# Kernel tuning notes

Hardware: AMD Instinct MI355X
Metric: run time of the kernel (lower is better)

Reference implementation:

```python
import jax, jax.numpy as jnp
import numpy as np

N = 100000
E = 3200000
IN_C, HID_C, OUT_C = 602, 256, 41
K = 10
ALPHA = 0.1
CLIP = 1000000.0


def _ntn(x):
    return jnp.nan_to_num(x, nan=0.0, posinf=CLIP, neginf=-CLIP)


def setup_inputs() -> dict:
    key = jax.random.key(0)
    k1, k2, k3, k4, k5 = jax.random.split(key, 5)
    x = jax.random.normal(k1, (N, IN_C), dtype=jnp.float32)
    edge_index = jax.random.randint(k2, (2, E), 0, N, dtype=jnp.int32)
    # Xavier-uniform linear weights (torch Linear: y = x @ W.T + b)
    lim1 = float(np.sqrt(6.0 / (IN_C + HID_C)))
    lim2 = float(np.sqrt(6.0 / (HID_C + OUT_C)))
    W1 = jax.random.uniform(k3, (HID_C, IN_C), jnp.float32, -lim1, lim1)
    W2 = jax.random.uniform(k4, (OUT_C, HID_C), jnp.float32, -lim2, lim2)
    b1 = jnp.zeros((HID_C,), jnp.float32)
    b2 = jnp.zeros((OUT_C,), jnp.float32)
    return {"x": x, "edge_index": edge_index, "W1": W1, "b1": b1, "W2": W2, "b2": b2}


def reference(x, edge_index, W1, b1, W2, b2):
    # MLP encoder (eval mode: dropout is identity)
    h = _ntn(x)
    h = jax.nn.relu(h @ W1.T + b1)
    h = _ntn(h)
    h = h @ W2.T + b2
    h = _ntn(h)

    # is_reddit path: L2-normalize rows before propagation
    h = h / jnp.maximum(jnp.linalg.norm(h, axis=1, keepdims=True), 1e-12)

    # APPNP with GCN normalization and added self-loops
    self_loop = jnp.arange(N, dtype=edge_index.dtype)
    row = jnp.concatenate([edge_index[0], self_loop])  # sources
    col = jnp.concatenate([edge_index[1], self_loop])  # targets
    deg = jax.ops.segment_sum(jnp.ones_like(col, dtype=h.dtype), col, num_segments=N)
    dinv = jax.lax.rsqrt(deg)  # deg >= 1 with self-loops
    norm = dinv[row] * dinv[col]  # [E+N]

    h0 = h

    def step(h_k, _):
        msg = h_k[row] * norm[:, None]  # gather + scale
        agg = jax.ops.segment_sum(msg, col, num_segments=N)  # scatter-add
        return (1.0 - ALPHA) * agg + ALPHA * h0, None

    out, _ = jax.lax.scan(step, h, None, length=K)
    out = _ntn(out)  # nan_to_num after prop (reddit path) and final nan_to_num
    return out
```

## Files before the change

kernel.cpp:

```cpp
#include <hip/hip_runtime.h>

#define N_NODES 100000
#define N_EDGES 3200000
#define IN_C 602
#define KPAD 608
#define NT 19
#define HID_C 256
#define OUTC 41
#define HSTR 64
#define K_ITERS 10
#define NBUK 391
#define NBLK_BIN 256
#define CHUNK 12500

typedef __attribute__((ext_vector_type(8))) short bf16x8;
typedef __attribute__((ext_vector_type(4))) float f32x4;

static __device__ __forceinline__ unsigned short f2bf(float f) {
  unsigned u = __float_as_uint(f);
  u += 0x7fffu + ((u >> 16) & 1u);
  return (unsigned short)(u >> 16);
}
static __device__ __forceinline__ float bf2f(unsigned short h) {
  return __uint_as_float(((unsigned)h) << 16);
}
static __device__ __forceinline__ float bflo(unsigned u) {
  return __uint_as_float(u << 16);
}
static __device__ __forceinline__ float bfhi(unsigned u) {
  return __uint_as_float(u & 0xffff0000u);
}
static __device__ __forceinline__ unsigned enc8(float v) {
  return (unsigned)(int)rintf(fminf(fmaxf(v * 127.f + 128.f, 0.f), 255.f));
}
static __device__ __forceinline__ unsigned pk4(float a, float b, float c, float d) {
  return enc8(a) | (enc8(b) << 8) | (enc8(c) << 16) | (enc8(d) << 24);
}

__global__ __launch_bounds__(256) void dinv_kernel(const unsigned* __restrict__ offs,
                                                   float* __restrict__ dinv) {
  int i = blockIdx.x * 256 + threadIdx.x;
  if (i < N_NODES) dinv[i] = rsqrtf((float)(offs[i + 1] - offs[i] + 1u));
}

__global__ __launch_bounds__(256) void binA_kernel(const int* __restrict__ col,
                                                   unsigned* __restrict__ gh) {
  __shared__ unsigned lh[NBUK];
  const int tid = threadIdx.x, blk = blockIdx.x;
  for (int i = tid; i < NBUK; i += 256) lh[i] = 0;
  __syncthreads();
  const int start = blk * CHUNK;
  const int end = (start + CHUNK < N_EDGES) ? start + CHUNK : N_EDGES;
  for (int e = start + tid; e < end; e += 256)
    atomicAdd(&lh[col[e] >> 8], 1u);
  __syncthreads();
  for (int i = tid; i < NBUK; i += 256)
    gh[(size_t)i * NBLK_BIN + blk] = lh[i];
}

__global__ __launch_bounds__(512) void binScan_kernel(unsigned* __restrict__ gh,
                                                      unsigned* __restrict__ bbase2,
                                                      unsigned* __restrict__ bhist) {
  __shared__ unsigned wsum[8];
  __shared__ unsigned wbase[8];
  const int t = threadIdx.x, lane = t & 63, w = t >> 6;
  unsigned tot = 0;
  if (t < NBUK) {
    unsigned* gp = gh + (size_t)t * NBLK_BIN;
#pragma unroll 8
    for (int j = 0; j < NBLK_BIN; ++j) tot += gp[j];
  }
  unsigned inc = tot;
  for (int d = 1; d < 64; d <<= 1) {
    unsigned x = (unsigned)__shfl_up((int)inc, d);
    if (lane >= d) inc += x;
  }
  if (lane == 63) wsum[w] = inc;
  __syncthreads();
  if (t == 0) {
    unsigned run = 0;
    for (int i = 0; i < 8; ++i) { unsigned s = wsum[i]; wbase[i] = run; run += s; }
  }
  __syncthreads();
  if (t < NBUK) {
    unsigned base = wbase[w] + inc - tot;
    bbase2[t] = base;
    bhist[t] = tot;
    unsigned* gp = gh + (size_t)t * NBLK_BIN;
    unsigned run = base;
#pragma unroll 8
    for (int j = 0; j < NBLK_BIN; ++j) {
      unsigned v = gp[j];
      gp[j] = run;
      run += v;
    }
  }
}

__global__ __launch_bounds__(256) void binB_kernel(const int* __restrict__ row,
                                                   const int* __restrict__ col,
                                                   const unsigned* __restrict__ gh,
                                                   unsigned* __restrict__ binned) {
  __shared__ unsigned lbase[NBUK];
  __shared__ unsigned lcur[NBUK];
  const int tid = threadIdx.x, blk = blockIdx.x;
  for (int i = tid; i < NBUK; i += 256) {
    lbase[i] = gh[(size_t)i * NBLK_BIN + blk];
    lcur[i] = 0;
  }
  __syncthreads();
  const int start = blk * CHUNK;
  const int end = (start + CHUNK < N_EDGES) ? start + CHUNK : N_EDGES;
  for (int e = start + tid; e < end; e += 256) {
    int r = row[e], c = col[e];
    int b = c >> 8;
    unsigned idx = atomicAdd(&lcur[b], 1u);
    binned[lbase[b] + idx] = (((unsigned)(c & 255)) << 17) | (unsigned)r;
  }
}

__global__ __launch_bounds__(256) void place_kernel(const unsigned* __restrict__ binned,
                                                    const unsigned* __restrict__ bbase2,
                                                    const unsigned* __restrict__ bhist,
                                                    unsigned* __restrict__ offs,
                                                    unsigned* __restrict__ rec4) {
  __shared__ unsigned lcnt[256];
  __shared__ unsigned lbase[256];
  __shared__ unsigned lcur[256];
  __shared__ unsigned wsum[4];
  __shared__ unsigned wbase[4];
  const int tid = threadIdx.x, lane = tid & 63, w = tid >> 6;
  const int b = blockIdx.x;
  const unsigned s = bbase2[b];
  const unsigned cnt = bhist[b];
  lcnt[tid] = 0;
  __syncthreads();
  for (unsigned i = tid; i < cnt; i += 256)
    atomicAdd(&lcnt[binned[s + i] >> 17], 1u);
  __syncthreads();
  unsigned v = lcnt[tid];
  unsigned inc = v;
  for (int d = 1; d < 64; d <<= 1) {
    unsigned x = (unsigned)__shfl_up((int)inc, d);
    if (lane >= d) inc += x;
  }
  if (lane == 63) wsum[w] = inc;
  __syncthreads();
  if (tid == 0) {
    unsigned run = 0;
    for (int j = 0; j < 4; ++j) { unsigned t = wsum[j]; wbase[j] = run; run += t; }
  }
  __syncthreads();
  unsigned ex = wbase[w] + inc - v;
  lbase[tid] = ex;
  lcur[tid] = 0;
  const int node = (b << 8) + tid;
  if (node < N_NODES) offs[node] = s + ex;
  if (b == 0 && tid == 0) offs[N_NODES] = N_EDGES;
  __syncthreads();
  for (unsigned i = tid; i < cnt; i += 256) {
    unsigned pv = binned[s + i];
    unsigned cI = pv >> 17;
    unsigned pos = atomicAdd(&lcur[cI], 1u);
    rec4[s + lbase[cI] + pos] = pv & 0x1FFFFu;
  }
}

__global__ __launch_bounds__(256) void wprep1_kernel(const float* __restrict__ W1,
                                                     unsigned short* __restrict__ Whf) {
  int idx = blockIdx.x * 256 + threadIdx.x;
  if (idx >= HID_C * KPAD) return;
  int n = idx / KPAD, k = idx % KPAD;
  float v = (k < IN_C) ? W1[n * IN_C + k] : 0.f;
  int t = k >> 5, g = (k >> 3) & 3, j = k & 7;
  Whf[(size_t)t * 8192 + (((n << 2) + g) << 3) + j] = f2bf(v);
}

__global__ __launch_bounds__(256) void wprep2_kernel(const float* __restrict__ W2,
                                                     unsigned short* __restrict__ W2hf,
                                                     unsigned short* __restrict__ W2lf) {
  int idx = blockIdx.x * 256 + threadIdx.x;
  if (idx >= 48 * HID_C) return;
  int n = idx >> 8, k = idx & 255;
  float v = (n < OUTC) ? W2[n * HID_C + k] : 0.f;
  unsigned short hi = f2bf(v);
  int ks = k >> 5, g = (k >> 3) & 3, j = k & 7;
  size_t dst = (size_t)ks * 1536 + (((n << 2) + g) << 3) + j;
  W2hf[dst] = hi;
  W2lf[dst] = f2bf(v - bf2f(hi));
}

__global__ __launch_bounds__(256, 4) void gemm1_kernel(
    const float* __restrict__ x,
    const unsigned short* __restrict__ Whf,
    const float* __restrict__ b1,
    unsigned short* __restrict__ h1g) {
  __shared__ __align__(16) char smem[16896];
  float4* xt = (float4*)smem;
  unsigned short* h1t = (unsigned short*)smem;

  const int tid = threadIdx.x;
  const int lane = tid & 63;
  const int w = tid >> 6;
  const int r0 = blockIdx.x * 32;
  const int fr = lane & 15;
  const int g = lane >> 4;

  const int srow = tid >> 3;
  const int sc = tid & 7;
  int gr0 = r0 + srow;
  if (gr0 >= N_NODES) gr0 = N_NODES - 1;
  const float* xp0 = x + (size_t)gr0 * IN_C;
  const int ws0 = srow * 8 + (sc ^ (srow & 7));

  f32x4 acc[2][4];
  {
    const int bcol0 = (w << 6) + fr;
#pragma unroll
    for (int s = 0; s < 4; ++s) {
      float bv = b1[bcol0 + s * 16];
#pragma unroll
      for (int mi = 0; mi < 2; ++mi) acc[mi][s] = (f32x4){bv, bv, bv, bv};
    }
  }

  float4 pA0, pB0;
  bf16x8 bhv[2][4];

#define STAGE_LOAD0(T)                                                     \
  { const int kb = (T) * 32 + sc * 4;                                      \
    if ((T) < NT - 1) { pA0 = *(const float4*)(xp0 + kb); }                \
    else { float t0[4];                                                    \
      _Pragma("unroll") for (int j = 0; j < 4; ++j) { int k = kb + j;      \
        t0[j] = (k < IN_C) ? xp0[k] : 0.f; }                               \
      pA0 = (float4){t0[0], t0[1], t0[2], t0[3]}; } }

#define STAGE_LOAD1(T)                                                     \
  { const int kb = (T) * 32 + sc * 4;                                      \
    if ((T) < NT - 1) { pB0 = *(const float4*)(xp0 + kb); }                \
    else { float t0[4];                                                    \
      _Pragma("unroll") for (int j = 0; j < 4; ++j) { int k = kb + j;      \
        t0[j] = (k < IN_C) ? xp0[k] : 0.f; }                               \
      pB0 = (float4){t0[0], t0[1], t0[2], t0[3]}; } }

#define STAGE_WRITE0(BW) { xt[(BW) * 256 + ws0] = pA0; }
#define STAGE_WRITE1(BW) { xt[(BW) * 256 + ws0] = pB0; }

#define LOADB(T, PAR)                                                      \
  { const size_t tb = (size_t)(T) * 8192;                                  \
    _Pragma("unroll") for (int s = 0; s < 4; ++s) {                        \
      const int n4 = (((w << 6) + s * 16 + fr) << 2) + g;                  \
      bhv[PAR][s] = *(const bf16x8*)(Whf + tb + n4 * 8);                   \
    } }

#define COMPUTE(BR, PAR)                                                   \
  { _Pragma("unroll") for (int mi = 0; mi < 2; ++mi) {                     \
      const int rr = mi * 16 + fr;                                         \
      float4 pa = xt[(BR) * 256 + rr * 8 + ((2 * g) ^ (fr & 7))];          \
      float4 pb = xt[(BR) * 256 + rr * 8 + ((2 * g + 1) ^ (fr & 7))];      \
      union { unsigned u[4]; bf16x8 v; } hh, ll;                           \
      asm("v_cvt_pk_bf16_f32 %0, %1, %2" : "=v"(hh.u[0]) : "v"(pa.x), "v"(pa.y)); \
      asm("v_cvt_pk_bf16_f32 %0, %1, %2" : "=v"(hh.u[1]) : "v"(pa.z), "v"(pa.w)); \
      asm("v_cvt_pk_bf16_f32 %0, %1, %2" : "=v"(hh.u[2]) : "v"(pb.x), "v"(pb.y)); \
      asm("v_cvt_pk_bf16_f32 %0, %1, %2" : "=v"(hh.u[3]) : "v"(pb.z), "v"(pb.w)); \
      float l0 = pa.x - bflo(hh.u[0]), l1 = pa.y - bfhi(hh.u[0]);          \
      float l2 = pa.z - bflo(hh.u[1]), l3 = pa.w - bfhi(hh.u[1]);          \
      float l4 = pb.x - bflo(hh.u[2]), l5 = pb.y - bfhi(hh.u[2]);          \
      float l6 = pb.z - bflo(hh.u[3]), l7 = pb.w - bfhi(hh.u[3]);          \
      asm("v_cvt_pk_bf16_f32 %0, %1, %2" : "=v"(ll.u[0]) : "v"(l0), "v"(l1)); \
      asm("v_cvt_pk_bf16_f32 %0, %1, %2" : "=v"(ll.u[1]) : "v"(l2), "v"(l3)); \
      asm("v_cvt_pk_bf16_f32 %0, %1, %2" : "=v"(ll.u[2]) : "v"(l4), "v"(l5)); \
      asm("v_cvt_pk_bf16_f32 %0, %1, %2" : "=v"(ll.u[3]) : "v"(l6), "v"(l7)); \
      _Pragma("unroll") for (int s = 0; s < 4; ++s) {                      \
        acc[mi][s] = __builtin_amdgcn_mfma_f32_16x16x32_bf16(              \
            hh.v, bhv[PAR][s], acc[mi][s], 0, 0, 0);                       \
        acc[mi][s] = __builtin_amdgcn_mfma_f32_16x16x32_bf16(              \
            ll.v, bhv[PAR][s], acc[mi][s], 0, 0, 0);                       \
      } } }

#define BODY(T, PAR)                                                       \
  { int bW = bR + 1; if (bW == 3) bW = 0;                                  \
    if ((T) + 1 < NT) {                                                    \
      if ((PAR) == 0) STAGE_WRITE1(bW) else STAGE_WRITE0(bW);              \
      if ((T) + 3 < NT) { if ((PAR) == 0) STAGE_LOAD1((T) + 3)             \
                          else STAGE_LOAD0((T) + 3); }                     \
      LOADB((T) + 1, (PAR) ^ 1);                                           \
    }                                                                      \
    COMPUTE(bR, PAR);                                                      \
    __syncthreads();                                                       \
    bR = bW; }

  STAGE_LOAD0(0);
  STAGE_WRITE0(0);
  STAGE_LOAD1(1);
  STAGE_LOAD0(2);
  LOADB(0, 0);
  __syncthreads();

  int bR = 0;
  for (int t = 0; t + 1 < NT; t += 2) {
    BODY(t, 0);
    BODY(t + 1, 1);
  }
  BODY(NT - 1, 0);

#pragma unroll
  for (int mi = 0; mi < 2; ++mi)
#pragma unroll
    for (int s = 0; s < 4; ++s)
#pragma unroll
      for (int q = 0; q < 4; ++q) {
        int rr = mi * 16 + (g << 2) + q;
        int cc = (w << 6) + s * 16 + fr;
        h1t[rr * 264 + cc] = f2bf(fmaxf(acc[mi][s][q], 0.f));
      }
  __syncthreads();
  {
    const int row = tid >> 3, seg = tid & 7;
    const int gr = r0 + row;
    if (gr < N_NODES) {
      const uint4* src = (const uint4*)&h1t[row * 264 + seg * 32];
      uint4* dst = (uint4*)(h1g + (size_t)gr * 256 + seg * 32);
      dst[0] = src[0];
      dst[1] = src[1];
      dst[2] = src[2];
      dst[3] = src[3];
    }
  }
}

__global__ __launch_bounds__(256) void gemm2_kernel(
    const unsigned short* __restrict__ h1g,
    const unsigned short* __restrict__ W2hf,
    const unsigned short* __restrict__ W2lf,
    const float* __restrict__ b2,
    unsigned short* __restrict__ H0) {
  const int tid = threadIdx.x;
  const int lane = tid & 63;
  const int w = tid >> 6;
  const int fr = lane & 15;
  const int g = lane >> 4;
  const int wr0 = blockIdx.x * 64 + w * 16;

  f32x4 acc[3];
#pragma unroll
  for (int s = 0; s < 3; ++s) {
    int c = s * 16 + fr;
    float bv = (c < OUTC) ? b2[c] : 0.f;
    acc[s] = (f32x4){bv, bv, bv, bv};
  }

  int ar = wr0 + fr;
  if (ar >= N_NODES) ar = N_NODES - 1;
  const unsigned short* ap = h1g + (size_t)ar * 256 + g * 8;

#pragma unroll
  for (int ks = 0; ks < 8; ++ks) {
    bf16x8 a = *(const bf16x8*)(ap + ks * 32);
#pragma unroll
    for (int s = 0; s < 3; ++s) {
      const int n4 = (((s * 16 + fr) << 2) + g) << 3;
      bf16x8 bh = *(const bf16x8*)(W2hf + (size_t)ks * 1536 + n4);
      bf16x8 bl = *(const bf16x8*)(W2lf + (size_t)ks * 1536 + n4);
      acc[s] = __builtin_amdgcn_mfma_f32_16x16x32_bf16(a, bh, acc[s], 0, 0, 0);
      acc[s] = __builtin_amdgcn_mfma_f32_16x16x32_bf16(a, bl, acc[s], 0, 0, 0);
    }
  }

  float ps[4];
#pragma unroll
  for (int q = 0; q < 4; ++q)
    ps[q] = acc[0][q] * acc[0][q] + acc[1][q] * acc[1][q] + acc[2][q] * acc[2][q];
#pragma unroll
  for (int m = 1; m < 16; m <<= 1)
#pragma unroll
    for (int q = 0; q < 4; ++q) ps[q] += __shfl_xor(ps[q], m);

#pragma unroll
  for (int q = 0; q < 4; ++q) {
    const int gr = wr0 + (g << 2) + q;
    if (gr < N_NODES) {
      float rn = 1.f / fmaxf(sqrtf(ps[q]), 1e-12f);
#pragma unroll
      for (int s = 0; s < 3; ++s)
        H0[(size_t)gr * HSTR + s * 16 + fr] = f2bf(acc[s][q] * rn);
      H0[(size_t)gr * HSTR + 48 + fr] = 0;
    }
  }
}

__global__ __launch_bounds__(256) void cvt8_kernel(const unsigned* __restrict__ h0b,
                                                   const float* __restrict__ dinv,
                                                   unsigned* __restrict__ h0f) {
  int idx = blockIdx.x * 256 + threadIdx.x;
  if (idx >= N_NODES * 16) return;
  int n = idx >> 4, j = idx & 15;
  unsigned out;
  if (j == 12) {
    out = __float_as_uint(dinv[n]);
  } else {
    unsigned a = h0b[(size_t)n * 32 + 2 * j];
    unsigned b = h0b[(size_t)n * 32 + 2 * j + 1];
    out = pk4(bflo(a), bfhi(a), bflo(b), bfhi(b));
  }
  h0f[idx] = out;
}

__global__ __launch_bounds__(256) void prop_kernel(
    const unsigned* __restrict__ hsrc,
    const unsigned* __restrict__ h0b,
    unsigned* __restrict__ hdst,
    float* __restrict__ fout,
    const unsigned* __restrict__ rec4,
    const unsigned* __restrict__ offs) {
  const int lane = threadIdx.x & 63;
  const int wv = threadIdx.x >> 6;
  const int sub = lane & 7;
  const int n = blockIdx.x * 32 + wv * 8 + (lane >> 3);
  if (n >= N_NODES) return;
  const int sf = (lane & 56) + 6;
  const unsigned s = offs[n];
  const unsigned e = offs[n + 1];
  const uint2* hs = (const uint2*)hsrc;
  float a0 = 0.f, a1 = 0.f, a2 = 0.f, a3 = 0.f;
  float a4 = 0.f, a5 = 0.f, a6 = 0.f, a7 = 0.f;
  float c0 = 0.f, c1 = 0.f, c2 = 0.f, c3 = 0.f;
  float c4 = 0.f, c5 = 0.f, c6 = 0.f, c7 = 0.f;
  float wsum = 0.f;

#define ACCU(U, W, P)                                                     \
  { float f0, f1, f2, f3, f4, f5, f6, f7;                                 \
    asm("v_cvt_f32_ubyte0 %0, %1" : "=v"(f0) : "v"((U).x));               \
    asm("v_cvt_f32_ubyte1 %0, %1" : "=v"(f1) : "v"((U).x));               \
    asm("v_cvt_f32_ubyte2 %0, %1" : "=v"(f2) : "v"((U).x));               \
    asm("v_cvt_f32_ubyte3 %0, %1" : "=v"(f3) : "v"((U).x));               \
    asm("v_cvt_f32_ubyte0 %0, %1" : "=v"(f4) : "v"((U).y));               \
    asm("v_cvt_f32_ubyte1 %0, %1" : "=v"(f5) : "v"((U).y));               \
    asm("v_cvt_f32_ubyte2 %0, %1" : "=v"(f6) : "v"((U).y));               \
    asm("v_cvt_f32_ubyte3 %0, %1" : "=v"(f7) : "v"((U).y));               \
    P##0 += f0 * (W); P##1 += f1 * (W);                                   \
    P##2 += f2 * (W); P##3 += f3 * (W);                                   \
    P##4 += f4 * (W); P##5 += f5 * (W);                                   \
    P##6 += f6 * (W); P##7 += f7 * (W);                                   \
    wsum += (W); }

  uint2 su = hs[(size_t)n * 8 + sub];
  float dn = __uint_as_float(__shfl((int)su.x, sf));

  unsigned i = s;
  for (; i + 8 <= e; i += 8) {
    unsigned r0 = rec4[i],     r1 = rec4[i + 1], r2 = rec4[i + 2], r3 = rec4[i + 3];
    unsigned r4 = rec4[i + 4], r5 = rec4[i + 5], r6 = rec4[i + 6], r7 = rec4[i + 7];
    uint2 u0 = hs[(size_t)r0 * 8 + sub];
    uint2 u1 = hs[(size_t)r1 * 8 + sub];
    uint2 u2 = hs[(size_t)r2 * 8 + sub];
    uint2 u3 = hs[(size_t)r3 * 8 + sub];
    uint2 u4 = hs[(size_t)r4 * 8 + sub];
    uint2 u5 = hs[(size_t)r5 * 8 + sub];
    uint2 u6 = hs[(size_t)r6 * 8 + sub];
    uint2 u7 = hs[(size_t)r7 * 8 + sub];
    float d0 = __uint_as_float(__shfl((int)u0.x, sf));
    float d1 = __uint_as_float(__shfl((int)u1.x, sf));
    float d2 = __uint_as_float(__shfl((int)u2.x, sf));
    float d3 = __uint_as_float(__shfl((int)u3.x, sf));
    float d4 = __uint_as_float(__shfl((int)u4.x, sf));
    float d5 = __uint_as_float(__shfl((int)u5.x, sf));
    float d6 = __uint_as_float(__shfl((int)u6.x, sf));
    float d7 = __uint_as_float(__shfl((int)u7.x, sf));
    ACCU(u0, d0, a);
    ACCU(u1, d1, c);
    ACCU(u2, d2, a);
    ACCU(u3, d3, c);
    ACCU(u4, d4, a);
    ACCU(u5, d5, c);
    ACCU(u6, d6, a);
    ACCU(u7, d7, c);
  }
  for (; i < e; ++i) {
    unsigned r = rec4[i];
    uint2 u = hs[(size_t)r * 8 + sub];
    float d = __uint_as_float(__shfl((int)u.x, sf));
    ACCU(u, d, a);
  }
  ACCU(su, dn, a);

  uint4 hv = ((const uint4*)h0b)[(size_t)n * 8 + sub];
  const float sc9 = 0.9f * dn * (1.f / 127.f);
  const float base = -128.f * sc9 * wsum;
  float o0 = sc9 * (a0 + c0) + base + 0.1f * bflo(hv.x);
  float o1 = sc9 * (a1 + c1) + base + 0.1f * bfhi(hv.x);
  float o2 = sc9 * (a2 + c2) + base + 0.1f * bflo(hv.y);
  float o3 = sc9 * (a3 + c3) + base + 0.1f * bfhi(hv.y);
  float o4 = sc9 * (a4 + c4) + base + 0.1f * bflo(hv.z);
  float o5 = sc9 * (a5 + c5) + base + 0.1f * bfhi(hv.z);
  float o6 = sc9 * (a6 + c6) + base + 0.1f * bflo(hv.w);
  float o7 = sc9 * (a7 + c7) + base + 0.1f * bfhi(hv.w);
  if (fout) {
    int cb = 8 * sub;
    if (cb < OUTC)     fout[(size_t)n * OUTC + cb] = o0;
    if (cb + 1 < OUTC) fout[(size_t)n * OUTC + cb + 1] = o1;
    if (cb + 2 < OUTC) fout[(size_t)n * OUTC + cb + 2] = o2;
    if (cb + 3 < OUTC) fout[(size_t)n * OUTC + cb + 3] = o3;
    if (cb + 4 < OUTC) fout[(size_t)n * OUTC + cb + 4] = o4;
    if (cb + 5 < OUTC) fout[(size_t)n * OUTC + cb + 5] = o5;
    if (cb + 6 < OUTC) fout[(size_t)n * OUTC + cb + 6] = o6;
    if (cb + 7 < OUTC) fout[(size_t)n * OUTC + cb + 7] = o7;
  } else {
    uint2 ow;
    ow.x = pk4(o0, o1, o2, o3);
    ow.y = pk4(o4, o5, o6, o7);
    if (sub == 6) ow.x = __float_as_uint(dn);
    ((uint2*)hdst)[(size_t)n * 8 + sub] = ow;
  }
}

extern "C" void kernel_launch(void* const* d_in, const int* in_sizes, int n_in,
                              void* d_out, int out_size, void* d_ws, size_t ws_size,
                              hipStream_t stream) {
  const float* x  = (const float*)d_in[0];
  const int*   ei = (const int*)d_in[1];
  const float* W1 = (const float*)d_in[2];
  const float* b1 = (const float*)d_in[3];
  const float* W2 = (const float*)d_in[4];
  const float* b2 = (const float*)d_in[5];
  float* out = (float*)d_out;

  char* p = (char*)d_ws;
  auto alloc = [&](size_t bytes) {
    char* q = p;
    p += (bytes + 255) & ~(size_t)255;
    return q;
  };
  float*    dinv   = (float*)   alloc((size_t)N_NODES * 4);
  unsigned* offs   = (unsigned*)alloc(((size_t)N_NODES + 1) * 4);
  unsigned* bhist  = (unsigned*)alloc((NBUK + 1) * 4);
  unsigned* bbase2 = (unsigned*)alloc((NBUK + 1) * 4);
  unsigned* gh     = (unsigned*)alloc((size_t)NBUK * NBLK_BIN * 4);
  unsigned* binned = (unsigned*)alloc((size_t)N_EDGES * 4);
  unsigned* rec4   = (unsigned*)alloc((size_t)N_EDGES * 4);
  unsigned short* H0b = (unsigned short*)alloc((size_t)N_NODES * HSTR * 2);
  unsigned* H0f = (unsigned*)alloc((size_t)N_NODES * 16 * 4);
  unsigned* HA  = (unsigned*)alloc((size_t)N_NODES * 16 * 4);
  unsigned* HB  = (unsigned*)alloc((size_t)N_NODES * 16 * 4);
  unsigned short* h1g = (unsigned short*)alloc((size_t)N_NODES * HID_C * 2);
  unsigned short* Whf = (unsigned short*)alloc((size_t)NT * 8192 * 2);
  unsigned short* W2hf = (unsigned short*)alloc((size_t)8 * 1536 * 2);
  unsigned short* W2lf = (unsigned short*)alloc((size_t)8 * 1536 * 2);

  const int* row = ei;
  const int* col = ei + N_EDGES;

  binA_kernel<<<NBLK_BIN, 256, 0, stream>>>(col, gh);
  binScan_kernel<<<1, 512, 0, stream>>>(gh, bbase2, bhist);
  binB_kernel<<<NBLK_BIN, 256, 0, stream>>>(row, col, gh, binned);
  place_kernel<<<NBUK, 256, 0, stream>>>(binned, bbase2, bhist, offs, rec4);
  dinv_kernel<<<(N_NODES + 255) / 256, 256, 0, stream>>>(offs, dinv);

  wprep1_kernel<<<(HID_C * KPAD + 255) / 256, 256, 0, stream>>>(W1, Whf);
  wprep2_kernel<<<(48 * HID_C + 255) / 256, 256, 0, stream>>>(W2, W2hf, W2lf);
  gemm1_kernel<<<(N_NODES + 31) / 32, 256, 0, stream>>>(x, Whf, b1, h1g);
  gemm2_kernel<<<(N_NODES + 63) / 64, 256, 0, stream>>>(h1g, W2hf, W2lf, b2, H0b);
  cvt8_kernel<<<(N_NODES * 16 + 255) / 256, 256, 0, stream>>>((const unsigned*)H0b, dinv, H0f);

  const unsigned* src = H0f;
  unsigned* bufs[2] = {HA, HB};
  for (int k = 0; k < K_ITERS; ++k) {
    bool last = (k == K_ITERS - 1);
    unsigned* dst = last ? nullptr : bufs[k & 1];
    float* fdst = last ? out : nullptr;
    prop_kernel<<<(N_NODES + 31) / 32, 256, 0, stream>>>(
        src, (const unsigned*)H0b, dst, fdst, rec4, offs);
    src = dst;
  }
}
```

Measured before the change: 713.5 us.

## Pre-pack x into MFMA-fragment bf16 layout and split W1 into hi/lo

Adds an xprep kernel that converts x to bf16 once and stores it in the exact per-lane MFMA fragment order, so gemm1 loads A operands straight from global memory with no LDS staging, no per-iteration barriers and no in-loop conversion. The split-precision correction moves from the activation side (x hi/lo) to the weight side (W1 hi/lo). gemm1 now handles 64-row tiles with 4x4 accumulators at lower occupancy. The cost is an extra full pass writing and then reading a bf16 copy of x, roughly 120MB of added traffic, and x is now rounded to a single bf16 with no low-part correction, which lowers accuracy.

```diff
diff --git a/kernel.cpp b/kernel.cpp
--- a/kernel.cpp
+++ b/kernel.cpp
@@ -5,6 +5,7 @@
 #define IN_C 602
 #define KPAD 608
 #define NT 19
+#define NTILE 1563
 #define HID_C 256
 #define OUTC 41
 #define HSTR 64
@@ -166,14 +167,50 @@
   }
 }
 
+__global__ __launch_bounds__(256) void xprep_kernel(const float* __restrict__ x,
+                                                    unsigned short* __restrict__ xf) {
+  const int b = blockIdx.x;
+  const int nt = b / NT, t = b - nt * NT;
+  const int tid = threadIdx.x;
+  const int r = tid >> 2;
+  const int kc = tid & 3;
+  int gr = nt * 64 + r;
+  if (gr >= N_NODES) gr = N_NODES - 1;
+  const int kb = t * 32 + kc * 8;
+  const float* xp = x + (size_t)gr * IN_C + kb;
+  float v[8];
+  if (kb + 8 <= IN_C) {
+    float4 p0 = *(const float4*)xp;
+    float4 p1 = *(const float4*)(xp + 4);
+    v[0] = p0.x; v[1] = p0.y; v[2] = p0.z; v[3] = p0.w;
+    v[4] = p1.x; v[5] = p1.y; v[6] = p1.z; v[7] = p1.w;
+  } else {
+#pragma unroll
+    for (int j = 0; j < 8; ++j) {
+      int k = kb + j;
+      v[j] = (k < IN_C) ? xp[j] : 0.f;
+    }
+  }
+  union { unsigned short u[8]; bf16x8 v8; } pk;
+#pragma unroll
+  for (int j = 0; j < 8; ++j) pk.u[j] = f2bf(v[j]);
+  const int mi = r >> 4;
+  const int lane2 = (r & 15) | (kc << 4);
+  *(bf16x8*)(xf + ((size_t)(b * 4 + mi) * 512 + lane2 * 8)) = pk.v8;
+}
+
 __global__ __launch_bounds__(256) void wprep1_kernel(const float* __restrict__ W1,
-                                                     unsigned short* __restrict__ Whf) {
+                                                     unsigned short* __restrict__ Whf,
+                                                     unsigned short* __restrict__ Wlf) {
   int idx = blockIdx.x * 256 + threadIdx.x;
   if (idx >= HID_C * KPAD) return;
   int n = idx / KPAD, k = idx % KPAD;
   float v = (k < IN_C) ? W1[n * IN_C + k] : 0.f;
+  unsigned short hi = f2bf(v);
   int t = k >> 5, g = (k >> 3) & 3, j = k & 7;
-  Whf[(size_t)t * 8192 + (((n << 2) + g) << 3) + j] = f2bf(v);
+  size_t dst = (size_t)t * 8192 + (((n << 2) + g) << 3) + j;
+  Whf[dst] = hi;
+  Wlf[dst] = f2bf(v - bf2f(hi));
 }
 
 __global__ __launch_bounds__(256) void wprep2_kernel(const float* __restrict__ W2,
@@ -190,122 +227,73 @@
   W2lf[dst] = f2bf(v - bf2f(hi));
 }
 
-__global__ __launch_bounds__(256, 4) void gemm1_kernel(
-    const float* __restrict__ x,
+__global__ __launch_bounds__(256, 2) void gemm1_kernel(
+    const unsigned short* __restrict__ xf,
     const unsigned short* __restrict__ Whf,
+    const unsigned short* __restrict__ Wlf,
     const float* __restrict__ b1,
     unsigned short* __restrict__ h1g) {
-  __shared__ __align__(16) char smem[16896];
-  float4* xt = (float4*)smem;
-  unsigned short* h1t = (unsigned short*)smem;
+  __shared__ unsigned short h1t[64 * 264];
 
   const int tid = threadIdx.x;
   const int lane = tid & 63;
   const int w = tid >> 6;
-  const int r0 = blockIdx.x * 32;
+  const int nt = blockIdx.x;
+  const int r0 = nt * 64;
   const int fr = lane & 15;
   const int g = lane >> 4;
 
-  const int srow = tid >> 3;
-  const int sc = tid & 7;
-  int gr0 = r0 + srow;
-  if (gr0 >= N_NODES) gr0 = N_NODES - 1;
-  const float* xp0 = x + (size_t)gr0 * IN_C;
-  const int ws0 = srow * 8 + (sc ^ (srow & 7));
-
-  f32x4 acc[2][4];
+  f32x4 acc[4][4];
   {
     const int bcol0 = (w << 6) + fr;
 #pragma unroll
     for (int s = 0; s < 4; ++s) {
       float bv = b1[bcol0 + s * 16];
 #pragma unroll
-      for (int mi = 0; mi < 2; ++mi) acc[mi][s] = (f32x4){bv, bv, bv, bv};
-    }
-  }
-
-  float4 pA0, pB0;
-  bf16x8 bhv[2][4];
-
-#define STAGE_LOAD0(T)                                                     \
-  { const int kb = (T) * 32 + sc * 4;                                      \
-    if ((T) < NT - 1) { pA0 = *(const float4*)(xp0 + kb); }                \
-    else { float t0[4];                                                    \
-      _Pragma("unroll") for (int j = 0; j < 4; ++j) { int k = kb + j;      \
-        t0[j] = (k < IN_C) ? xp0[k] : 0.f; }                               \
-      pA0 = (float4){t0[0], t0[1], t0[2], t0[3]}; } }
-
-#define STAGE_LOAD1(T)                                                     \
-  { const int kb = (T) * 32 + sc * 4;                                      \
-    if ((T) < NT - 1) { pB0 = *(const float4*)(xp0 + kb); }                \
-    else { float t0[4];                                                    \
-      _Pragma("unroll") for (int j = 0; j < 4; ++j) { int k = kb + j;      \
-        t0[j] = (k < IN_C) ? xp0[k] : 0.f; }                               \
-      pB0 = (float4){t0[0], t0[1], t0[2], t0[3]}; } }
-
-#define STAGE_WRITE0(BW) { xt[(BW) * 256 + ws0] = pA0; }
-#define STAGE_WRITE1(BW) { xt[(BW) * 256 + ws0] = pB0; }
-
-#define LOADB(T, PAR)                                                      \
+      for (int mi = 0; mi < 4; ++mi) acc[mi][s] = (f32x4){bv, bv, bv, bv};
+    }
+  }
+
+  const unsigned short* xb = xf + (size_t)nt * (NT * 2048);
+  bf16x8 aA[4], aB[4], bhA[4], blA[4], bhB[4], blB[4];
+
+#define LDA(T, A)                                                          \
+  { _Pragma("unroll") for (int mi = 0; mi < 4; ++mi)                       \
+      A[mi] = *(const bf16x8*)(xb + ((size_t)((T) * 4 + mi) * 512 + lane * 8)); }
+
+#define LDB(T, BH, BL)                                                     \
   { const size_t tb = (size_t)(T) * 8192;                                  \
     _Pragma("unroll") for (int s = 0; s < 4; ++s) {                        \
       const int n4 = (((w << 6) + s * 16 + fr) << 2) + g;                  \
-      bhv[PAR][s] = *(const bf16x8*)(Whf + tb + n4 * 8);                   \
+      BH[s] = *(const bf16x8*)(Whf + tb + n4 * 8);                         \
+      BL[s] = *(const bf16x8*)(Wlf + tb + n4 * 8);                         \
     } }
 
-#define COMPUTE(BR, PAR)                                                   \
-  { _Pragma("unroll") for (int mi = 0; mi < 2; ++mi) {                     \
-      const int rr = mi * 16 + fr;                                         \
-      float4 pa = xt[(BR) * 256 + rr * 8 + ((2 * g) ^ (fr & 7))];          \
-      float4 pb = xt[(BR) * 256 + rr * 8 + ((2 * g + 1) ^ (fr & 7))];      \
-      union { unsigned u[4]; bf16x8 v; } hh, ll;                           \
-      asm("v_cvt_pk_bf16_f32 %0, %1, %2" : "=v"(hh.u[0]) : "v"(pa.x), "v"(pa.y)); \
-      asm("v_cvt_pk_bf16_f32 %0, %1, %2" : "=v"(hh.u[1]) : "v"(pa.z), "v"(pa.w)); \
-      asm("v_cvt_pk_bf16_f32 %0, %1, %2" : "=v"(hh.u[2]) : "v"(pb.x), "v"(pb.y)); \
-      asm("v_cvt_pk_bf16_f32 %0, %1, %2" : "=v"(hh.u[3]) : "v"(pb.z), "v"(pb.w)); \
-      float l0 = pa.x - bflo(hh.u[0]), l1 = pa.y - bfhi(hh.u[0]);          \
-      float l2 = pa.z - bflo(hh.u[1]), l3 = pa.w - bfhi(hh.u[1]);          \
-      float l4 = pb.x - bflo(hh.u[2]), l5 = pb.y - bfhi(hh.u[2]);          \
-      float l6 = pb.z - bflo(hh.u[3]), l7 = pb.w - bfhi(hh.u[3]);          \
-      asm("v_cvt_pk_bf16_f32 %0, %1, %2" : "=v"(ll.u[0]) : "v"(l0), "v"(l1)); \
-      asm("v_cvt_pk_bf16_f32 %0, %1, %2" : "=v"(ll.u[1]) : "v"(l2), "v"(l3)); \
-      asm("v_cvt_pk_bf16_f32 %0, %1, %2" : "=v"(ll.u[2]) : "v"(l4), "v"(l5)); \
-      asm("v_cvt_pk_bf16_f32 %0, %1, %2" : "=v"(ll.u[3]) : "v"(l6), "v"(l7)); \
+#define MM(A, BH, BL)                                                      \
+  { _Pragma("unroll") for (int mi = 0; mi < 4; ++mi)                       \
       _Pragma("unroll") for (int s = 0; s < 4; ++s) {                      \
         acc[mi][s] = __builtin_amdgcn_mfma_f32_16x16x32_bf16(              \
-            hh.v, bhv[PAR][s], acc[mi][s], 0, 0, 0);                       \
+            A[mi], BH[s], acc[mi][s], 0, 0, 0);                            \
         acc[mi][s] = __builtin_amdgcn_mfma_f32_16x16x32_bf16(              \
-            ll.v, bhv[PAR][s], acc[mi][s], 0, 0, 0);                       \
-      } } }
-
-#define BODY(T, PAR)                                                       \
-  { int bW = bR + 1; if (bW == 3) bW = 0;                                  \
-    if ((T) + 1 < NT) {                                                    \
-      if ((PAR) == 0) STAGE_WRITE1(bW) else STAGE_WRITE0(bW);              \
-      if ((T) + 3 < NT) { if ((PAR) == 0) STAGE_LOAD1((T) + 3)             \
-                          else STAGE_LOAD0((T) + 3); }                     \
-      LOADB((T) + 1, (PAR) ^ 1);                                           \
-    }                                                                      \
-    COMPUTE(bR, PAR);                                                      \
-    __syncthreads();                                                       \
-    bR = bW; }
-
-  STAGE_LOAD0(0);
-  STAGE_WRITE0(0);
-  STAGE_LOAD1(1);
-  STAGE_LOAD0(2);
-  LOADB(0, 0);
-  __syncthreads();
-
-  int bR = 0;
+            A[mi], BL[s], acc[mi][s], 0, 0, 0);                            \
+      } }
+
+  LDA(0, aA);
+  LDB(0, bhA, blA);
   for (int t = 0; t + 1 < NT; t += 2) {
-    BODY(t, 0);
-    BODY(t + 1, 1);
-  }
-  BODY(NT - 1, 0);
-
-#pragma unroll
-  for (int mi = 0; mi < 2; ++mi)
+    LDA(t + 1, aB);
+    LDB(t + 1, bhB, blB);
+    MM(aA, bhA, blA);
+    if (t + 2 < NT) {
+      LDA(t + 2, aA);
+      LDB(t + 2, bhA, blA);
+    }
+    MM(aB, bhB, blB);
+  }
+  MM(aA, bhA, blA);
+
+#pragma unroll
+  for (int mi = 0; mi < 4; ++mi)
 #pragma unroll
     for (int s = 0; s < 4; ++s)
 #pragma unroll
@@ -316,15 +304,13 @@
       }
   __syncthreads();
   {
-    const int row = tid >> 3, seg = tid & 7;
+    const int row = tid >> 2, seg = tid & 3;
     const int gr = r0 + row;
     if (gr < N_NODES) {
-      const uint4* src = (const uint4*)&h1t[row * 264 + seg * 32];
-      uint4* dst = (uint4*)(h1g + (size_t)gr * 256 + seg * 32);
-      dst[0] = src[0];
-      dst[1] = src[1];
-      dst[2] = src[2];
-      dst[3] = src[3];
+      const uint4* src = (const uint4*)&h1t[row * 264 + seg * 64];
+      uint4* dst = (uint4*)(h1g + (size_t)gr * 256 + seg * 64);
+#pragma unroll
+      for (int j = 0; j < 8; ++j) dst[j] = src[j];
     }
   }
 }
@@ -543,7 +529,9 @@
   unsigned* HA  = (unsigned*)alloc((size_t)N_NODES * 16 * 4);
   unsigned* HB  = (unsigned*)alloc((size_t)N_NODES * 16 * 4);
   unsigned short* h1g = (unsigned short*)alloc((size_t)N_NODES * HID_C * 2);
+  unsigned short* xf  = (unsigned short*)alloc((size_t)NTILE * NT * 2048 * 2);
   unsigned short* Whf = (unsigned short*)alloc((size_t)NT * 8192 * 2);
+  unsigned short* Wlf = (unsigned short*)alloc((size_t)NT * 8192 * 2);
   unsigned short* W2hf = (unsigned short*)alloc((size_t)8 * 1536 * 2);
   unsigned short* W2lf = (unsigned short*)alloc((size_t)8 * 1536 * 2);
 
@@ -556,9 +544,10 @@
   place_kernel<<<NBUK, 256, 0, stream>>>(binned, bbase2, bhist, offs, rec4);
   dinv_kernel<<<(N_NODES + 255) / 256, 256, 0, stream>>>(offs, dinv);
 
-  wprep1_kernel<<<(HID_C * KPAD + 255) / 256, 256, 0, stream>>>(W1, Whf);
+  xprep_kernel<<<NTILE * NT, 256, 0, stream>>>(x, xf);
+  wprep1_kernel<<<(HID_C * KPAD + 255) / 256, 256, 0, stream>>>(W1, Whf, Wlf);
   wprep2_kernel<<<(48 * HID_C + 255) / 256, 256, 0, stream>>>(W2, W2hf, W2lf);
-  gemm1_kernel<<<(N_NODES + 31) / 32, 256, 0, stream>>>(x, Whf, b1, h1g);
+  gemm1_kernel<<<NTILE, 256, 0, stream>>>(xf, Whf, Wlf, b1, h1g);
   gemm2_kernel<<<(N_NODES + 63) / 64, 256, 0, stream>>>(h1g, W2hf, W2lf, b2, H0b);
   cvt8_kernel<<<(N_NODES * 16 + 255) / 256, 256, 0, stream>>>((const unsigned*)H0b, dinv, H0f);
 
```

Result: slower. 780.3 us (+9.4%).
